# Optimization experiments

Hardware: AMD Instinct MI355X
Metric: run time of the kernel (lower is better)

Reference implementation:

```python
import jax, jax.numpy as jnp
import numpy as np

N_U = 50000; N_I = 50000; F = 128; H = 128; E = 800000; G = 512; C = 16; L = 3
EPS = 1e-5


def setup_inputs() -> dict:
    key = jax.random.key(0)
    ks = jax.random.split(key, 22)
    s = 1.0 / np.sqrt(H)
    inp = {}
    inp["x_user"] = jax.random.normal(ks[0], (N_U, F), jnp.float32)
    inp["x_item"] = jax.random.normal(ks[1], (N_I, F), jnp.float32)
    inp["edge_u2i"] = jnp.stack([jax.random.randint(ks[2], (E,), 0, N_U),
                                 jax.random.randint(ks[3], (E,), 0, N_I)])
    inp["edge_i2u"] = jnp.stack([jax.random.randint(ks[4], (E,), 0, N_I),
                                 jax.random.randint(ks[5], (E,), 0, N_U)])
    inp["batch_user"] = jnp.sort(jax.random.randint(ks[6], (N_U,), 0, G))
    inp["batch_item"] = jnp.sort(jax.random.randint(ks[7], (N_I,), 0, G))
    # GraphConv params per layer per relation (in-dim == hidden == 128, so stackable)
    inp["Wrel_u2i"] = jax.random.uniform(ks[8], (L, H, F), jnp.float32, -s, s)
    inp["Wroot_u2i"] = jax.random.uniform(ks[9], (L, H, F), jnp.float32, -s, s)
    inp["b_u2i"] = jax.random.uniform(ks[10], (L, H), jnp.float32, -s, s)
    inp["Wrel_i2u"] = jax.random.uniform(ks[11], (L, H, F), jnp.float32, -s, s)
    inp["Wroot_i2u"] = jax.random.uniform(ks[12], (L, H, F), jnp.float32, -s, s)
    inp["b_i2u"] = jax.random.uniform(ks[13], (L, H), jnp.float32, -s, s)
    # BatchNorm (one module per node type, reused across layers)
    inp["bn_g_user"] = jnp.ones((H,), jnp.float32)
    inp["bn_b_user"] = jnp.zeros((H,), jnp.float32)
    inp["bn_g_item"] = jnp.ones((H,), jnp.float32)
    inp["bn_b_item"] = jnp.zeros((H,), jnp.float32)
    # per-layer classifier heads
    inp["fc_W"] = jax.random.uniform(ks[14], (L, C, H), jnp.float32, -s, s)
    inp["fc_b"] = jax.random.uniform(ks[15], (L, C), jnp.float32, -s, s)
    return inp


def _graph_conv(x_src, x_dst, edge, Wrel, Wroot, b, n_dst):
    # GraphConv, aggr='add': W_rel @ sum_{j in N(i)} x_j + W_root @ x_i + b
    agg = jax.ops.segment_sum(x_src[edge[0]], edge[1], num_segments=n_dst)  # [n_dst, F]
    return agg @ Wrel.T + x_dst @ Wroot.T + b


def _bn(x, g, b):
    # BatchNorm1d over nodes, training-mode batch statistics (biased var)
    m = x.mean(0)
    v = jnp.mean((x - m) ** 2, axis=0)
    return (x - m) * jax.lax.rsqrt(v + EPS) * g + b


def reference(x_user, x_item, edge_u2i, edge_i2u, batch_user, batch_item,
              Wrel_u2i, Wroot_u2i, b_u2i, Wrel_i2u, Wroot_i2u, b_i2u,
              bn_g_user, bn_b_user, bn_g_item, bn_b_item, fc_W, fc_b):
    batch_all = jnp.concatenate([batch_user, batch_item])
    cnt = jax.ops.segment_sum(jnp.ones((N_U + N_I,), jnp.float32), batch_all,
                              num_segments=G)
    cnt = jnp.maximum(cnt, 1.0)[:, None]
    feats = []
    xu, xi = x_user, x_item
    for l in range(L):
        new_i = _graph_conv(xu, xi, edge_u2i, Wrel_u2i[l], Wroot_u2i[l], b_u2i[l], N_I)
        new_u = _graph_conv(xi, xu, edge_i2u, Wrel_i2u[l], Wroot_i2u[l], b_i2u[l], N_U)
        xu = _bn(jax.nn.relu(new_u), bn_g_user, bn_b_user)
        xi = _bn(jax.nn.relu(new_i), bn_g_item, bn_b_item)
        pooled = jax.ops.segment_sum(jnp.concatenate([xu, xi], 0), batch_all,
                                     num_segments=G) / cnt  # global mean pool [G, H]
        feats.append(pooled)
    feats = jnp.stack(feats)  # [L, G, H]
    # eval mode: F.dropout is identity; per-layer linear heads
    logits = jnp.einsum('lgh,lch->lgc', feats, fc_W) + fc_b[:, None, :]  # [L, G, C]
    return (logits, feats)
```

## Files before the change

### kernel.cpp

```cpp
#include <hip/hip_runtime.h>

#define NN 50000
#define FD 128
#define NE 800000
#define NG 512
#define NC 16
#define NL 3
#define NTOT 100000
#define NBLK 391
#define NBUCK 196
#define CAP 10240
#define BINTILE 2048
#define NBINBLK 782
#define BNEPS 1e-5f
#define LOGITS_N (NL*NG*NC)

typedef unsigned short u16;
typedef unsigned char u8;
typedef __attribute__((ext_vector_type(8))) short short8;
typedef __attribute__((ext_vector_type(4))) float f32x4;

#define OFF_GCNT     0ul
#define OFF_BCUR     4096ul
#define OFF_ACC      5120ul
#define MEMSET_BYTES 7168ul
#define OFF_USTART   7680ul
#define OFF_ISTART   10240ul
#define OFF_INVCNT   12800ul
#define OFF_BNSC     14848ul
#define OFF_BNSH     15872ul
#define OFF_ROWRANGE 16896ul
#define OFF_WB       817152ul
#define OFF_CSR      1210368ul
#define OFF_AGGI     9238528ul
#define OFF_AGGU     22038528ul
#define OFF_XU       34838528ul
#define OFF_XI       47638528ul
#define OFF_XU0      60438528ul
#define OFF_XI0      73238528ul

static __device__ __forceinline__ float bf2f(u16 v) {
  return __uint_as_float(((unsigned)v) << 16);
}
static __device__ __forceinline__ u16 f2bf(float f) {
  unsigned u = __float_as_uint(f);
  return (u16)((u + 0x7FFFu + ((u >> 16) & 1u)) >> 16);
}
static __device__ __forceinline__ void acc8(float* a, int4 v) {
  a[0] += __uint_as_float(((unsigned)v.x) << 16);
  a[1] += __uint_as_float(((unsigned)v.x) & 0xffff0000u);
  a[2] += __uint_as_float(((unsigned)v.y) << 16);
  a[3] += __uint_as_float(((unsigned)v.y) & 0xffff0000u);
  a[4] += __uint_as_float(((unsigned)v.z) << 16);
  a[5] += __uint_as_float(((unsigned)v.z) & 0xffff0000u);
  a[6] += __uint_as_float(((unsigned)v.w) << 16);
  a[7] += __uint_as_float(((unsigned)v.w) & 0xffff0000u);
}
static __device__ __forceinline__ void unp8(float* a, int4 v) {
  a[0] = __uint_as_float(((unsigned)v.x) << 16);
  a[1] = __uint_as_float(((unsigned)v.x) & 0xffff0000u);
  a[2] = __uint_as_float(((unsigned)v.y) << 16);
  a[3] = __uint_as_float(((unsigned)v.y) & 0xffff0000u);
  a[4] = __uint_as_float(((unsigned)v.z) << 16);
  a[5] = __uint_as_float(((unsigned)v.z) & 0xffff0000u);
  a[6] = __uint_as_float(((unsigned)v.w) << 16);
  a[7] = __uint_as_float(((unsigned)v.w) & 0xffff0000u);
}

__global__ __launch_bounds__(256) void k_hist_batch(const int* __restrict__ bu,
                                                    const int* __restrict__ bi,
                                                    int* __restrict__ gcnt) {
  int i = blockIdx.x*256 + threadIdx.x;
  if (i >= NTOT) return;
  int type = i >= NN;
  int g = type ? bi[i-NN] : bu[i];
  atomicAdd(&gcnt[type*NG + g], 1);
}

__global__ __launch_bounds__(512) void k_scan_g(const int* __restrict__ gcnt,
                                                int* __restrict__ ustart,
                                                int* __restrict__ istart,
                                                float* __restrict__ invcnt) {
  __shared__ int pu[512], pi[512];
  int t = threadIdx.x;
  int cu = gcnt[t], ci = gcnt[NG + t];
  pu[t] = cu; pi[t] = ci;
  __syncthreads();
  for (int off = 1; off < 512; off <<= 1) {
    int vu = (t >= off) ? pu[t-off] : 0;
    int vi = (t >= off) ? pi[t-off] : 0;
    __syncthreads();
    pu[t] += vu; pi[t] += vi;
    __syncthreads();
  }
  ustart[t] = pu[t] - cu;
  istart[t] = pi[t] - ci;
  if (t == 511) { ustart[NG] = pu[511]; istart[NG] = pi[511]; }
  int c = cu + ci;
  invcnt[t] = 1.0f / (float)(c > 0 ? c : 1);
}

__global__ __launch_bounds__(256) void k_bin(const int* __restrict__ eu2i,
                                             const int* __restrict__ ei2u,
                                             int* __restrict__ bcursor,
                                             int* __restrict__ binned) {
  __shared__ int hist[256];
  __shared__ int scan[256];
  __shared__ int gbase[256];
  __shared__ int rbuf[BINTILE];
  __shared__ u8 rbk[BINTILE];
  int tid = threadIdx.x;
  int base = blockIdx.x * BINTILE;
  hist[tid] = 0;
  __syncthreads();
  int packr[8], bkr[8], rankr[8];
  #pragma unroll
  for (int c = 0; c < 8; c++) {
    int idx = base + c*256 + tid;
    if (idx < 2*NE) {
      int rel = idx >= NE;
      int e = rel ? idx - NE : idx;
      const int* edge = rel ? ei2u : eu2i;
      int s = edge[e];
      int d = edge[NE + e];
      int slot = d + (rel ? NN : 0);
      int bk = slot >> 9;
      bkr[c] = bk;
      packr[c] = ((slot & 511) << 17) | s;
      rankr[c] = atomicAdd(&hist[bk], 1);
    } else bkr[c] = -1;
  }
  __syncthreads();
  scan[tid] = hist[tid];
  __syncthreads();
  for (int o = 1; o < 256; o <<= 1) {
    int v = (tid >= o) ? scan[tid - o] : 0;
    __syncthreads();
    scan[tid] += v;
    __syncthreads();
  }
  if (tid < NBUCK && hist[tid] > 0)
    gbase[tid] = atomicAdd(&bcursor[tid], hist[tid]);
  __syncthreads();
  #pragma unroll
  for (int c = 0; c < 8; c++) {
    if (bkr[c] >= 0) {
      int bk = bkr[c];
      int lpos = scan[bk] - hist[bk] + rankr[c];
      rbuf[lpos] = packr[c];
      rbk[lpos] = (u8)bk;
    }
  }
  __syncthreads();
  int nv = min(BINTILE, 2*NE - base);
  for (int j = tid; j < nv; j += 256) {
    int bk = rbk[j];
    int outpos = bk*CAP + gbase[bk] + (j - (scan[bk] - hist[bk]));
    binned[outpos] = rbuf[j];
  }
}

__global__ __launch_bounds__(256) void k_csrbuild(const int* __restrict__ bcursor,
                                                  int* __restrict__ csrbin,
                                                  int2* __restrict__ rowrange) {
  __shared__ int lcnt[512];
  __shared__ int scan2[256];
  __shared__ int lcsr[CAP];
  int b = blockIdx.x;
  int tid = threadIdx.x;
  int slot0 = b << 9;
  int nslots = min(512, NTOT - slot0);
  int n = bcursor[b];
  int gb = b * CAP;
  lcnt[tid] = 0; lcnt[tid + 256] = 0;
  __syncthreads();
  for (int i = tid; i < n; i += 256) {
    int e = csrbin[gb + i];
    atomicAdd(&lcnt[e >> 17], 1);
  }
  __syncthreads();
  int v0 = lcnt[2*tid], v1 = lcnt[2*tid + 1];
  int ps = v0 + v1;
  scan2[tid] = ps;
  __syncthreads();
  for (int o = 1; o < 256; o <<= 1) {
    int v = (tid >= o) ? scan2[tid - o] : 0;
    __syncthreads();
    scan2[tid] += v;
    __syncthreads();
  }
  int e0 = scan2[tid] - ps;
  int e1 = e0 + v0;
  if (2*tid < nslots)     rowrange[slot0 + 2*tid]     = make_int2(gb + e0, gb + e0 + v0);
  if (2*tid + 1 < nslots) rowrange[slot0 + 2*tid + 1] = make_int2(gb + e1, gb + e1 + v1);
  __syncthreads();
  lcnt[2*tid] = e0; lcnt[2*tid + 1] = e1;
  __syncthreads();
  for (int i = tid; i < n; i += 256) {
    int e = csrbin[gb + i];
    int pos = atomicAdd(&lcnt[e >> 17], 1);
    lcsr[pos] = e & 0x1FFFF;
  }
  __syncthreads();
  for (int i = tid; i < n; i += 256) csrbin[gb + i] = lcsr[i];
}

__global__ __launch_bounds__(256) void k_castX(const float* __restrict__ xu,
                                               const float* __restrict__ xi,
                                               u16* __restrict__ xbu,
                                               u16* __restrict__ xbi) {
  int b = blockIdx.x;
  int half = b >= 6250;
  const float* src = half ? xi : xu;
  u16* dst = half ? xbi : xbu;
  int i = ((half ? b - 6250 : b)*256 + threadIdx.x) * 4;
  float4 v = *(const float4*)(src + i);
  ushort4 o = { f2bf(v.x), f2bf(v.y), f2bf(v.z), f2bf(v.w) };
  *(ushort4*)(dst + i) = o;
}

__global__ __launch_bounds__(256) void k_castW(const float* __restrict__ WrelA,
                                               const float* __restrict__ WrootA,
                                               const float* __restrict__ WrelB,
                                               const float* __restrict__ WrootB,
                                               u16* __restrict__ WB) {
  int idx = blockIdx.x*256 + threadIdx.x;
  int lr = idx >> 15;
  int rem = idx & 32767;
  int h = rem >> 8;
  int k = rem & 255;
  int l = lr >> 1;
  int rel = lr & 1;
  const float* Wr = rel ? WrelB : WrelA;
  const float* Wo = rel ? WrootB : WrootA;
  float v = (k < FD) ? Wr[(l*FD + h)*FD + k] : Wo[(l*FD + h)*FD + (k-FD)];
  WB[idx] = f2bf(v);
}

__global__ __launch_bounds__(256) void k_gather(const u16* __restrict__ curU,
                                                const u16* __restrict__ curI,
                                                const int2* __restrict__ rowrange,
                                                const int* __restrict__ csr,
                                                u16* __restrict__ aggI,
                                                u16* __restrict__ aggU) {
  int b = blockIdx.x;
  int half = b >= 12500;
  int blk = half ? b - 12500 : b;
  const u16* src = half ? curI : curU;
  u16* out = half ? aggU : aggI;
  int slotbase = half ? NN : 0;
  int wid = __builtin_amdgcn_readfirstlane(threadIdx.x >> 6);
  int row = blk*4 + wid;
  int lane = threadIdx.x & 63;
  int q = lane >> 4;
  int c16 = (lane & 15) * 8;
  const u16* sp = src + c16;
  int2 pr = rowrange[slotbase + row];
  int p = pr.x, pe = pr.y;
  float a0[8], a1[8];
  #pragma unroll
  for (int j = 0; j < 8; j++) { a0[j] = 0.f; a1[j] = 0.f; }
  if (p + 8 <= pe) {
    int i0 = csr[p + q], i1 = csr[p + 4 + q];
    while (p + 16 <= pe) {
      int n0 = csr[p + 8 + q], n1 = csr[p + 12 + q];
      int4 v0 = *(const int4*)(sp + (size_t)i0*FD);
      int4 v1 = *(const int4*)(sp + (size_t)i1*FD);
      acc8(a0, v0); acc8(a1, v1);
      i0 = n0; i1 = n1; p += 8;
    }
    int4 v0 = *(const int4*)(sp + (size_t)i0*FD);
    int4 v1 = *(const int4*)(sp + (size_t)i1*FD);
    acc8(a0, v0); acc8(a1, v1);
    p += 8;
  }
  int rem = pe - p;
  if (q < rem) {
    int s = csr[p + q];
    acc8(a0, *(const int4*)(sp + (size_t)s*FD));
  }
  if (q + 4 < rem) {
    int s = csr[p + 4 + q];
    acc8(a1, *(const int4*)(sp + (size_t)s*FD));
  }
  #pragma unroll
  for (int j = 0; j < 8; j++) a0[j] += a1[j];
  #pragma unroll
  for (int j = 0; j < 8; j++) {
    a0[j] += __shfl_xor(a0[j], 16);
    a0[j] += __shfl_xor(a0[j], 32);
  }
  if (q == 0) {
    int4 o;
    o.x = (unsigned)f2bf(a0[0]) | ((unsigned)f2bf(a0[1]) << 16);
    o.y = (unsigned)f2bf(a0[2]) | ((unsigned)f2bf(a0[3]) << 16);
    o.z = (unsigned)f2bf(a0[4]) | ((unsigned)f2bf(a0[5]) << 16);
    o.w = (unsigned)f2bf(a0[6]) | ((unsigned)f2bf(a0[7]) << 16);
    *(int4*)(out + (size_t)row*FD + c16) = o;
  }
}

__global__ __launch_bounds__(256) void k_gemm(u16* __restrict__ aggU,
                                              u16* __restrict__ aggI,
                                              const u16* __restrict__ curU,
                                              const u16* __restrict__ curI,
                                              const u16* __restrict__ WBl,
                                              const float* __restrict__ bI2U,
                                              const float* __restrict__ bU2I,
                                              float* __restrict__ accSQ) {
  __shared__ u16 As[128*72];
  __shared__ u16 Bs[128*72];
  __shared__ float Sred[2][4][128];
  int ty = blockIdx.y;
  u16* A1 = ty ? aggI : aggU;
  const u16* A2 = ty ? curI : curU;
  const u16* WBp = ty ? WBl : (WBl + 32768);
  const float* bias = ty ? bU2I : bI2U;
  int tid = threadIdx.x;
  int n0 = blockIdx.x * 128;
  int w = __builtin_amdgcn_readfirstlane(tid >> 6);
  int lane = tid & 63;
  int l15 = lane & 15;
  int quad = lane >> 4;
  f32x4 acc[2][8];
  #pragma unroll
  for (int tr = 0; tr < 2; tr++)
    #pragma unroll
    for (int tc = 0; tc < 8; tc++)
      acc[tr][tc] = (f32x4){0.f,0.f,0.f,0.f};

  for (int ch = 0; ch < 4; ch++) {
    const u16* Ap = (ch < 2) ? ((const u16*)A1 + ch*64) : (A2 + (ch-2)*64);
    #pragma unroll
    for (int i = 0; i < 4; i++) {
      int e = i*256 + tid;
      int r = e >> 3, seg = e & 7;
      int4 v = {0,0,0,0};
      int gr = n0 + r;
      if (gr < NN) v = *(const int4*)(Ap + (size_t)gr*FD + seg*8);
      *(int4*)&As[r*72 + seg*8] = v;
    }
    #pragma unroll
    for (int i = 0; i < 4; i++) {
      int e = i*256 + tid;
      int r = e >> 3, seg = e & 7;
      int4 v = *(const int4*)(WBp + r*256 + ch*64 + seg*8);
      *(int4*)&Bs[r*72 + seg*8] = v;
    }
    __syncthreads();
    #pragma unroll
    for (int ks = 0; ks < 2; ks++) {
      int kb = ks*32 + quad*8;
      short8 af0 = *(const short8*)&As[(w*32 + l15)*72 + kb];
      short8 af1 = *(const short8*)&As[(w*32 + 16 + l15)*72 + kb];
      short8 bf[8];
      #pragma unroll
      for (int tc = 0; tc < 8; tc++)
        bf[tc] = *(const short8*)&Bs[(tc*16 + l15)*72 + kb];
      #pragma unroll
      for (int tc = 0; tc < 8; tc++) {
        acc[0][tc] = __builtin_amdgcn_mfma_f32_16x16x32_bf16(af0, bf[tc], acc[0][tc], 0, 0, 0);
        acc[1][tc] = __builtin_amdgcn_mfma_f32_16x16x32_bf16(af1, bf[tc], acc[1][tc], 0, 0, 0);
      }
    }
    __syncthreads();
  }
  float sv[8], qv[8], bj[8];
  #pragma unroll
  for (int tc = 0; tc < 8; tc++) {
    bj[tc] = bias[tc*16 + l15];
    sv[tc] = 0.f; qv[tc] = 0.f;
  }
  #pragma unroll
  for (int tr = 0; tr < 2; tr++) {
    int rbase = n0 + w*32 + tr*16 + quad*4;
    #pragma unroll
    for (int tc = 0; tc < 8; tc++) {
      int col = tc*16 + l15;
      #pragma unroll
      for (int g = 0; g < 4; g++) {
        int r = rbase + g;
        if (r < NN) {
          float v = acc[tr][tc][g] + bj[tc];
          float y = v > 0.f ? v : 0.f;
          sv[tc] += y; qv[tc] += y*y;
          A1[(size_t)r*FD + col] = f2bf(v);
        }
      }
    }
  }
  #pragma unroll
  for (int tc = 0; tc < 8; tc++) {
    sv[tc] += __shfl_xor(sv[tc], 16); qv[tc] += __shfl_xor(qv[tc], 16);
    sv[tc] += __shfl_xor(sv[tc], 32); qv[tc] += __shfl_xor(qv[tc], 32);
  }
  if (quad == 0) {
    #pragma unroll
    for (int tc = 0; tc < 8; tc++) {
      Sred[0][w][tc*16 + l15] = sv[tc];
      Sred[1][w][tc*16 + l15] = qv[tc];
    }
  }
  __syncthreads();
  if (tid < 128) {
    float s = Sred[0][0][tid] + Sred[0][1][tid] + Sred[0][2][tid] + Sred[0][3][tid];
    float q = Sred[1][0][tid] + Sred[1][1][tid] + Sred[1][2][tid] + Sred[1][3][tid];
    atomicAdd(&accSQ[ty*128 + tid], s);
    atomicAdd(&accSQ[256 + ty*128 + tid], q);
  }
}

__global__ __launch_bounds__(256) void k_bnfinal(float* __restrict__ accSQ,
                                                 const float* __restrict__ gu,
                                                 const float* __restrict__ bu,
                                                 const float* __restrict__ gi,
                                                 const float* __restrict__ bi,
                                                 float* __restrict__ bnsc,
                                                 float* __restrict__ bnsh) {
  int tid = threadIdx.x;
  int type = tid >> 7;
  int c = tid & 127;
  float s = accSQ[tid];
  float q = accSQ[256 + tid];
  accSQ[tid] = 0.f;
  accSQ[256 + tid] = 0.f;
  float inv = 1.0f / (float)NN;
  float mean = s * inv;
  float var = q * inv - mean*mean;
  float rstd = rsqrtf(var + BNEPS);
  float g = type ? gi[c] : gu[c];
  float bb = type ? bi[c] : bu[c];
  float sc = rstd * g;
  bnsc[tid] = sc;
  bnsh[tid] = bb - mean * sc;
}

__global__ __launch_bounds__(256) void k_bnpool(const u16* __restrict__ newU,
                                                const u16* __restrict__ newI,
                                                const int* __restrict__ ustart,
                                                const int* __restrict__ istart,
                                                const float* __restrict__ bnsc,
                                                const float* __restrict__ bnsh,
                                                const float* __restrict__ invcnt,
                                                u16* __restrict__ xu,
                                                u16* __restrict__ xi,
                                                float* __restrict__ feats) {
  __shared__ float red[16][128];
  int tid = threadIdx.x;
  int g = blockIdx.x;
  int rt = tid >> 4;
  int c8 = (tid & 15) * 8;
  float acc[8];
  #pragma unroll
  for (int j = 0; j < 8; j++) acc[j] = 0.f;
  #pragma unroll
  for (int type = 0; type < 2; type++) {
    const u16* in = type ? newI : newU;
    u16* out = type ? xi : xu;
    const int* st = type ? istart : ustart;
    int rs = st[g], re = st[g+1];
    float sc[8], sh[8];
    #pragma unroll
    for (int j = 0; j < 8; j++) {
      sc[j] = bnsc[type*128 + c8 + j];
      sh[j] = bnsh[type*128 + c8 + j];
    }
    int r = rs + rt;
    for (; r + 16 < re; r += 32) {
      int4 v0 = *(const int4*)(in + (size_t)r*FD + c8);
      int4 v1 = *(const int4*)(in + (size_t)(r+16)*FD + c8);
      float f0[8], f1[8];
      unp8(f0, v0); unp8(f1, v1);
      u16 ov[8];
      #pragma unroll
      for (int j = 0; j < 8; j++) {
        float y = f0[j] > 0.f ? f0[j] : 0.f;
        float o = y * sc[j] + sh[j];
        ov[j] = f2bf(o); acc[j] += o;
      }
      int4 ow;
      ow.x = (unsigned)ov[0] | ((unsigned)ov[1] << 16);
      ow.y = (unsigned)ov[2] | ((unsigned)ov[3] << 16);
      ow.z = (unsigned)ov[4] | ((unsigned)ov[5] << 16);
      ow.w = (unsigned)ov[6] | ((unsigned)ov[7] << 16);
      *(int4*)(out + (size_t)r*FD + c8) = ow;
      #pragma unroll
      for (int j = 0; j < 8; j++) {
        float y = f1[j] > 0.f ? f1[j] : 0.f;
        float o = y * sc[j] + sh[j];
        ov[j] = f2bf(o); acc[j] += o;
      }
      ow.x = (unsigned)ov[0] | ((unsigned)ov[1] << 16);
      ow.y = (unsigned)ov[2] | ((unsigned)ov[3] << 16);
      ow.z = (unsigned)ov[4] | ((unsigned)ov[5] << 16);
      ow.w = (unsigned)ov[6] | ((unsigned)ov[7] << 16);
      *(int4*)(out + (size_t)(r+16)*FD + c8) = ow;
    }
    for (; r < re; r += 16) {
      int4 v0 = *(const int4*)(in + (size_t)r*FD + c8);
      float f0[8];
      unp8(f0, v0);
      u16 ov[8];
      #pragma unroll
      for (int j = 0; j < 8; j++) {
        float y = f0[j] > 0.f ? f0[j] : 0.f;
        float o = y * sc[j] + sh[j];
        ov[j] = f2bf(o); acc[j] += o;
      }
      int4 ow;
      ow.x = (unsigned)ov[0] | ((unsigned)ov[1] << 16);
      ow.y = (unsigned)ov[2] | ((unsigned)ov[3] << 16);
      ow.z = (unsigned)ov[4] | ((unsigned)ov[5] << 16);
      ow.w = (unsigned)ov[6] | ((unsigned)ov[7] << 16);
      *(int4*)(out + (size_t)r*FD + c8) = ow;
    }
  }
  #pragma unroll
  for (int j = 0; j < 8; j++) red[rt][c8 + j] = acc[j];
  __syncthreads();
  if (tid < 128) {
    float s = 0.f;
    #pragma unroll
    for (int i = 0; i < 16; i++) s += red[i][tid];
    feats[(size_t)g*FD + tid] = s * invcnt[g];
  }
}

__global__ __launch_bounds__(256) void k_heads(const float* __restrict__ feats,
                                               const float* __restrict__ fcW,
                                               const float* __restrict__ fcb,
                                               float* __restrict__ logits) {
  int idx = blockIdx.x*256 + threadIdx.x;
  if (idx >= LOGITS_N) return;
  int l = idx >> 13;
  int rem = idx & 8191;
  int g = rem >> 4;
  int c = rem & 15;
  const float* f = feats + ((size_t)l*NG + g)*FD;
  const float* w = fcW + ((size_t)l*NC + c)*FD;
  float s = 0.f;
  #pragma unroll
  for (int k = 0; k < FD; k += 4) {
    float4 fv = *(const float4*)(f + k);
    float4 wv = *(const float4*)(w + k);
    s += fv.x*wv.x + fv.y*wv.y + fv.z*wv.z + fv.w*wv.w;
  }
  logits[idx] = s + fcb[l*NC + c];
}

extern "C" void kernel_launch(void* const* d_in, const int* in_sizes, int n_in,
                              void* d_out, int out_size, void* d_ws, size_t ws_size,
                              hipStream_t stream) {
  const float* x_user   = (const float*)d_in[0];
  const float* x_item   = (const float*)d_in[1];
  const int*   eu2i     = (const int*)d_in[2];
  const int*   ei2u     = (const int*)d_in[3];
  const int*   bu       = (const int*)d_in[4];
  const int*   bi       = (const int*)d_in[5];
  const float* Wrel_u2i = (const float*)d_in[6];
  const float* Wroot_u2i= (const float*)d_in[7];
  const float* b_u2i    = (const float*)d_in[8];
  const float* Wrel_i2u = (const float*)d_in[9];
  const float* Wroot_i2u= (const float*)d_in[10];
  const float* b_i2u    = (const float*)d_in[11];
  const float* bn_g_user= (const float*)d_in[12];
  const float* bn_b_user= (const float*)d_in[13];
  const float* bn_g_item= (const float*)d_in[14];
  const float* bn_b_item= (const float*)d_in[15];
  const float* fcW      = (const float*)d_in[16];
  const float* fcb      = (const float*)d_in[17];

  char* ws = (char*)d_ws;
  int*   gcnt   = (int*)(ws + OFF_GCNT);
  int*   bcursor= (int*)(ws + OFF_BCUR);
  float* accSQ  = (float*)(ws + OFF_ACC);
  int*   ustart = (int*)(ws + OFF_USTART);
  int*   istart = (int*)(ws + OFF_ISTART);
  float* invcnt = (float*)(ws + OFF_INVCNT);
  float* bnsc   = (float*)(ws + OFF_BNSC);
  float* bnsh   = (float*)(ws + OFF_BNSH);
  int2*  rowrange = (int2*)(ws + OFF_ROWRANGE);
  u16*   WB     = (u16*)(ws + OFF_WB);
  int*   csrbin = (int*)(ws + OFF_CSR);
  u16*   aggI   = (u16*)(ws + OFF_AGGI);
  u16*   aggU   = (u16*)(ws + OFF_AGGU);
  u16*   xu     = (u16*)(ws + OFF_XU);
  u16*   xi     = (u16*)(ws + OFF_XI);
  u16*   xu0    = (u16*)(ws + OFF_XU0);
  u16*   xi0    = (u16*)(ws + OFF_XI0);
  float* fout   = (float*)d_out;
  float* featsAll = fout + LOGITS_N;

  hipMemsetAsync(ws, 0, MEMSET_BYTES, stream);
  k_hist_batch<<<NBLK, 256, 0, stream>>>(bu, bi, gcnt);
  k_bin<<<NBINBLK, 256, 0, stream>>>(eu2i, ei2u, bcursor, csrbin);
  k_scan_g<<<1, 512, 0, stream>>>(gcnt, ustart, istart, invcnt);
  k_csrbuild<<<NBUCK, 256, 0, stream>>>(bcursor, csrbin, rowrange);
  k_castX<<<12500, 256, 0, stream>>>(x_user, x_item, xu0, xi0);
  k_castW<<<768, 256, 0, stream>>>(Wrel_u2i, Wroot_u2i, Wrel_i2u, Wroot_i2u, WB);

  const u16* curU = xu0;
  const u16* curI = xi0;
  for (int l = 0; l < NL; l++) {
    k_gather<<<25000, 256, 0, stream>>>(curU, curI, rowrange, csrbin, aggI, aggU);
    k_gemm<<<dim3(NBLK,2), 256, 0, stream>>>(aggU, aggI, curU, curI,
                                             WB + (size_t)l*2*32768,
                                             b_i2u + l*FD, b_u2i + l*FD,
                                             accSQ);
    k_bnfinal<<<1, 256, 0, stream>>>(accSQ, bn_g_user, bn_b_user,
                                     bn_g_item, bn_b_item, bnsc, bnsh);
    k_bnpool<<<NG, 256, 0, stream>>>(aggU, aggI, ustart, istart, bnsc, bnsh,
                                     invcnt, xu, xi,
                                     featsAll + (size_t)l*NG*FD);
    curU = xu; curI = xi;
  }
  k_heads<<<96, 256, 0, stream>>>(featsAll, fcW, fcb, fout);
}
```

Measured before the change: 515.7 us.

## Fuse neighbor gather into GEMM, fold BN finalize and heads into pooling

The CSR gather-sum is merged into the MFMA GEMM kernel. Each 64-row block aggregates its neighbor rows straight into shared memory, so the aggregated tensor no longer makes a round trip through global memory. The BN finalize step moves into the pooling kernel, using per-layer accumulator slots so no reset is needed, and the classifier heads are computed per graph in the same kernel. This removes several launches and one full global write plus read of the aggregated features per layer. In exchange, gather latency now serialises ahead of the GEMM inside each block, and the root-term A operand is read directly from global memory.

Result: slower. 561.0 us (+8.8%).

```diff
diff --git a/kernel.cpp b/kernel.cpp
--- a/kernel.cpp
+++ b/kernel.cpp
@@ -8,6 +8,7 @@
 #define NL 3
 #define NTOT 100000
 #define NBLK 391
+#define NGG 782
 #define NBUCK 196
 #define CAP 10240
 #define BINTILE 2048
@@ -23,21 +24,19 @@
 #define OFF_GCNT     0ul
 #define OFF_BCUR     4096ul
 #define OFF_ACC      5120ul
-#define MEMSET_BYTES 7168ul
-#define OFF_USTART   7680ul
-#define OFF_ISTART   10240ul
-#define OFF_INVCNT   12800ul
-#define OFF_BNSC     14848ul
-#define OFF_BNSH     15872ul
-#define OFF_ROWRANGE 16896ul
-#define OFF_WB       817152ul
-#define OFF_CSR      1210368ul
-#define OFF_AGGI     9238528ul
-#define OFF_AGGU     22038528ul
-#define OFF_XU       34838528ul
-#define OFF_XI       47638528ul
-#define OFF_XU0      60438528ul
-#define OFF_XI0      73238528ul
+#define MEMSET_BYTES 11264ul
+#define OFF_USTART   11776ul
+#define OFF_ISTART   14336ul
+#define OFF_INVCNT   16896ul
+#define OFF_ROWRANGE 19456ul
+#define OFF_WB       819712ul
+#define OFF_CSR      1213440ul
+#define OFF_AGGI     9241600ul
+#define OFF_AGGU     22041600ul
+#define OFF_XU       34841600ul
+#define OFF_XI       47641600ul
+#define OFF_XU0      60441600ul
+#define OFF_XI0      73241600ul
 
 static __device__ __forceinline__ float bf2f(u16 v) {
   return __uint_as_float(((unsigned)v) << 16);
@@ -237,109 +236,92 @@
   WB[idx] = f2bf(v);
 }
 
-__global__ __launch_bounds__(256) void k_gather(const u16* __restrict__ curU,
-                                                const u16* __restrict__ curI,
-                                                const int2* __restrict__ rowrange,
-                                                const int* __restrict__ csr,
-                                                u16* __restrict__ aggI,
-                                                u16* __restrict__ aggU) {
-  int b = blockIdx.x;
-  int half = b >= 12500;
-  int blk = half ? b - 12500 : b;
-  const u16* src = half ? curI : curU;
-  u16* out = half ? aggU : aggI;
-  int slotbase = half ? NN : 0;
-  int wid = __builtin_amdgcn_readfirstlane(threadIdx.x >> 6);
-  int row = blk*4 + wid;
-  int lane = threadIdx.x & 63;
-  int q = lane >> 4;
-  int c16 = (lane & 15) * 8;
-  const u16* sp = src + c16;
-  int2 pr = rowrange[slotbase + row];
-  int p = pr.x, pe = pr.y;
-  float a0[8], a1[8];
-  #pragma unroll
-  for (int j = 0; j < 8; j++) { a0[j] = 0.f; a1[j] = 0.f; }
-  if (p + 8 <= pe) {
-    int i0 = csr[p + q], i1 = csr[p + 4 + q];
-    while (p + 16 <= pe) {
-      int n0 = csr[p + 8 + q], n1 = csr[p + 12 + q];
-      int4 v0 = *(const int4*)(sp + (size_t)i0*FD);
-      int4 v1 = *(const int4*)(sp + (size_t)i1*FD);
-      acc8(a0, v0); acc8(a1, v1);
-      i0 = n0; i1 = n1; p += 8;
-    }
-    int4 v0 = *(const int4*)(sp + (size_t)i0*FD);
-    int4 v1 = *(const int4*)(sp + (size_t)i1*FD);
-    acc8(a0, v0); acc8(a1, v1);
-    p += 8;
-  }
-  int rem = pe - p;
-  if (q < rem) {
-    int s = csr[p + q];
-    acc8(a0, *(const int4*)(sp + (size_t)s*FD));
-  }
-  if (q + 4 < rem) {
-    int s = csr[p + 4 + q];
-    acc8(a1, *(const int4*)(sp + (size_t)s*FD));
-  }
-  #pragma unroll
-  for (int j = 0; j < 8; j++) a0[j] += a1[j];
-  #pragma unroll
-  for (int j = 0; j < 8; j++) {
-    a0[j] += __shfl_xor(a0[j], 16);
-    a0[j] += __shfl_xor(a0[j], 32);
-  }
-  if (q == 0) {
-    int4 o;
-    o.x = (unsigned)f2bf(a0[0]) | ((unsigned)f2bf(a0[1]) << 16);
-    o.y = (unsigned)f2bf(a0[2]) | ((unsigned)f2bf(a0[3]) << 16);
-    o.z = (unsigned)f2bf(a0[4]) | ((unsigned)f2bf(a0[5]) << 16);
-    o.w = (unsigned)f2bf(a0[6]) | ((unsigned)f2bf(a0[7]) << 16);
-    *(int4*)(out + (size_t)row*FD + c16) = o;
-  }
-}
-
-__global__ __launch_bounds__(256) void k_gemm(u16* __restrict__ aggU,
-                                              u16* __restrict__ aggI,
-                                              const u16* __restrict__ curU,
-                                              const u16* __restrict__ curI,
-                                              const u16* __restrict__ WBl,
-                                              const float* __restrict__ bI2U,
-                                              const float* __restrict__ bU2I,
-                                              float* __restrict__ accSQ) {
-  __shared__ u16 As[128*72];
+__global__ __launch_bounds__(256, 4) void k_gg(u16* __restrict__ aggU,
+                                               u16* __restrict__ aggI,
+                                               const u16* __restrict__ curU,
+                                               const u16* __restrict__ curI,
+                                               const int2* __restrict__ rowrange,
+                                               const int* __restrict__ csr,
+                                               const u16* __restrict__ WBl,
+                                               const float* __restrict__ bI2U,
+                                               const float* __restrict__ bU2I,
+                                               float* __restrict__ accSQ) {
+  __shared__ u16 As[64*136];
   __shared__ u16 Bs[128*72];
   __shared__ float Sred[2][4][128];
   int ty = blockIdx.y;
-  u16* A1 = ty ? aggI : aggU;
+  const u16* gsrc = ty ? curU : curI;
+  int slotbase = ty ? 0 : NN;
   const u16* A2 = ty ? curI : curU;
   const u16* WBp = ty ? WBl : (WBl + 32768);
   const float* bias = ty ? bU2I : bI2U;
+  u16* out = ty ? aggI : aggU;
+
   int tid = threadIdx.x;
-  int n0 = blockIdx.x * 128;
   int w = __builtin_amdgcn_readfirstlane(tid >> 6);
   int lane = tid & 63;
   int l15 = lane & 15;
-  int quad = lane >> 4;
-  f32x4 acc[2][8];
-  #pragma unroll
-  for (int tr = 0; tr < 2; tr++)
-    #pragma unroll
-    for (int tc = 0; tc < 8; tc++)
-      acc[tr][tc] = (f32x4){0.f,0.f,0.f,0.f};
-
+  int q = lane >> 4;
+  int n0 = blockIdx.x * 64;
+  int c16 = l15 * 8;
+  const u16* sp = gsrc + c16;
+
+  for (int rr = 0; rr < 16; rr++) {
+    int row = n0 + w*16 + rr;
+    float a0[8], a1[8];
+    #pragma unroll
+    for (int j = 0; j < 8; j++) { a0[j] = 0.f; a1[j] = 0.f; }
+    if (row < NN) {
+      int2 pr = rowrange[slotbase + row];
+      int p = pr.x, pe = pr.y;
+      if (p + 8 <= pe) {
+        int i0 = csr[p + q], i1 = csr[p + 4 + q];
+        while (p + 16 <= pe) {
+          int m0 = csr[p + 8 + q], m1 = csr[p + 12 + q];
+          int4 v0 = *(const int4*)(sp + (size_t)i0*FD);
+          int4 v1 = *(const int4*)(sp + (size_t)i1*FD);
+          acc8(a0, v0); acc8(a1, v1);
+          i0 = m0; i1 = m1; p += 8;
+        }
+        int4 v0 = *(const int4*)(sp + (size_t)i0*FD);
+        int4 v1 = *(const int4*)(sp + (size_t)i1*FD);
+        acc8(a0, v0); acc8(a1, v1);
+        p += 8;
+      }
+      int rem = pe - p;
+      if (q < rem) {
+        int s = csr[p + q];
+        acc8(a0, *(const int4*)(sp + (size_t)s*FD));
+      }
+      if (q + 4 < rem) {
+        int s = csr[p + 4 + q];
+        acc8(a1, *(const int4*)(sp + (size_t)s*FD));
+      }
+    }
+    #pragma unroll
+    for (int j = 0; j < 8; j++) a0[j] += a1[j];
+    #pragma unroll
+    for (int j = 0; j < 8; j++) {
+      a0[j] += __shfl_xor(a0[j], 16);
+      a0[j] += __shfl_xor(a0[j], 32);
+    }
+    if (q == 0) {
+      int4 o;
+      o.x = (unsigned)f2bf(a0[0]) | ((unsigned)f2bf(a0[1]) << 16);
+      o.y = (unsigned)f2bf(a0[2]) | ((unsigned)f2bf(a0[3]) << 16);
+      o.z = (unsigned)f2bf(a0[4]) | ((unsigned)f2bf(a0[5]) << 16);
+      o.w = (unsigned)f2bf(a0[6]) | ((unsigned)f2bf(a0[7]) << 16);
+      *(int4*)&As[(w*16 + rr)*136 + c16] = o;
+    }
+  }
+
+  f32x4 acc[8];
+  #pragma unroll
+  for (int tc = 0; tc < 8; tc++) acc[tc] = (f32x4){0.f,0.f,0.f,0.f};
+  int arow = n0 + w*16 + l15;
+  bool arok = arow < NN;
   for (int ch = 0; ch < 4; ch++) {
-    const u16* Ap = (ch < 2) ? ((const u16*)A1 + ch*64) : (A2 + (ch-2)*64);
-    #pragma unroll
-    for (int i = 0; i < 4; i++) {
-      int e = i*256 + tid;
-      int r = e >> 3, seg = e & 7;
-      int4 v = {0,0,0,0};
-      int gr = n0 + r;
-      if (gr < NN) v = *(const int4*)(Ap + (size_t)gr*FD + seg*8);
-      *(int4*)&As[r*72 + seg*8] = v;
-    }
+    if (ch) __syncthreads();
     #pragma unroll
     for (int i = 0; i < 4; i++) {
       int e = i*256 + tid;
@@ -350,42 +332,40 @@
     __syncthreads();
     #pragma unroll
     for (int ks = 0; ks < 2; ks++) {
-      int kb = ks*32 + quad*8;
-      short8 af0 = *(const short8*)&As[(w*32 + l15)*72 + kb];
-      short8 af1 = *(const short8*)&As[(w*32 + 16 + l15)*72 + kb];
-      short8 bf[8];
-      #pragma unroll
-      for (int tc = 0; tc < 8; tc++)
-        bf[tc] = *(const short8*)&Bs[(tc*16 + l15)*72 + kb];
+      int kb = ks*32 + q*8;
+      short8 af;
+      if (ch < 2) {
+        af = *(const short8*)&As[(w*16 + l15)*136 + ch*64 + kb];
+      } else {
+        af = (short8){0,0,0,0,0,0,0,0};
+        if (arok) af = *(const short8*)(A2 + (size_t)arow*FD + (ch-2)*64 + kb);
+      }
       #pragma unroll
       for (int tc = 0; tc < 8; tc++) {
-        acc[0][tc] = __builtin_amdgcn_mfma_f32_16x16x32_bf16(af0, bf[tc], acc[0][tc], 0, 0, 0);
-        acc[1][tc] = __builtin_amdgcn_mfma_f32_16x16x32_bf16(af1, bf[tc], acc[1][tc], 0, 0, 0);
-      }
-    }
-    __syncthreads();
-  }
+        short8 bf = *(const short8*)&Bs[(tc*16 + l15)*72 + kb];
+        acc[tc] = __builtin_amdgcn_mfma_f32_16x16x32_bf16(af, bf, acc[tc], 0, 0, 0);
+      }
+    }
+  }
+
   float sv[8], qv[8], bj[8];
   #pragma unroll
   for (int tc = 0; tc < 8; tc++) {
     bj[tc] = bias[tc*16 + l15];
     sv[tc] = 0.f; qv[tc] = 0.f;
   }
-  #pragma unroll
-  for (int tr = 0; tr < 2; tr++) {
-    int rbase = n0 + w*32 + tr*16 + quad*4;
-    #pragma unroll
-    for (int tc = 0; tc < 8; tc++) {
-      int col = tc*16 + l15;
-      #pragma unroll
-      for (int g = 0; g < 4; g++) {
-        int r = rbase + g;
-        if (r < NN) {
-          float v = acc[tr][tc][g] + bj[tc];
-          float y = v > 0.f ? v : 0.f;
-          sv[tc] += y; qv[tc] += y*y;
-          A1[(size_t)r*FD + col] = f2bf(v);
-        }
+  int rbase = n0 + w*16 + q*4;
+  #pragma unroll
+  for (int tc = 0; tc < 8; tc++) {
+    int col = tc*16 + l15;
+    #pragma unroll
+    for (int g = 0; g < 4; g++) {
+      int r = rbase + g;
+      if (r < NN) {
+        float v = acc[tc][g] + bj[tc];
+        float y = v > 0.f ? v : 0.f;
+        sv[tc] += y; qv[tc] += y*y;
+        out[(size_t)r*FD + col] = f2bf(v);
       }
     }
   }
@@ -394,7 +374,7 @@
     sv[tc] += __shfl_xor(sv[tc], 16); qv[tc] += __shfl_xor(qv[tc], 16);
     sv[tc] += __shfl_xor(sv[tc], 32); qv[tc] += __shfl_xor(qv[tc], 32);
   }
-  if (quad == 0) {
+  if (q == 0) {
     #pragma unroll
     for (int tc = 0; tc < 8; tc++) {
       Sred[0][w][tc*16 + l15] = sv[tc];
@@ -404,50 +384,49 @@
   __syncthreads();
   if (tid < 128) {
     float s = Sred[0][0][tid] + Sred[0][1][tid] + Sred[0][2][tid] + Sred[0][3][tid];
-    float q = Sred[1][0][tid] + Sred[1][1][tid] + Sred[1][2][tid] + Sred[1][3][tid];
+    float qq = Sred[1][0][tid] + Sred[1][1][tid] + Sred[1][2][tid] + Sred[1][3][tid];
     atomicAdd(&accSQ[ty*128 + tid], s);
-    atomicAdd(&accSQ[256 + ty*128 + tid], q);
-  }
-}
-
-__global__ __launch_bounds__(256) void k_bnfinal(float* __restrict__ accSQ,
-                                                 const float* __restrict__ gu,
-                                                 const float* __restrict__ bu,
-                                                 const float* __restrict__ gi,
-                                                 const float* __restrict__ bi,
-                                                 float* __restrict__ bnsc,
-                                                 float* __restrict__ bnsh) {
-  int tid = threadIdx.x;
-  int type = tid >> 7;
-  int c = tid & 127;
-  float s = accSQ[tid];
-  float q = accSQ[256 + tid];
-  accSQ[tid] = 0.f;
-  accSQ[256 + tid] = 0.f;
-  float inv = 1.0f / (float)NN;
-  float mean = s * inv;
-  float var = q * inv - mean*mean;
-  float rstd = rsqrtf(var + BNEPS);
-  float g = type ? gi[c] : gu[c];
-  float bb = type ? bi[c] : bu[c];
-  float sc = rstd * g;
-  bnsc[tid] = sc;
-  bnsh[tid] = bb - mean * sc;
+    atomicAdd(&accSQ[256 + ty*128 + tid], qq);
+  }
 }
 
 __global__ __launch_bounds__(256) void k_bnpool(const u16* __restrict__ newU,
                                                 const u16* __restrict__ newI,
                                                 const int* __restrict__ ustart,
                                                 const int* __restrict__ istart,
-                                                const float* __restrict__ bnsc,
-                                                const float* __restrict__ bnsh,
+                                                const float* __restrict__ accSQ,
+                                                const float* __restrict__ gu,
+                                                const float* __restrict__ bu,
+                                                const float* __restrict__ gi,
+                                                const float* __restrict__ bi,
                                                 const float* __restrict__ invcnt,
                                                 u16* __restrict__ xu,
                                                 u16* __restrict__ xi,
-                                                float* __restrict__ feats) {
+                                                float* __restrict__ feats,
+                                                const float* __restrict__ fcWl,
+                                                const float* __restrict__ fcbl,
+                                                float* __restrict__ logitsl) {
   __shared__ float red[16][128];
+  __shared__ float ssc[256], ssh[256];
+  __shared__ float sfeat[128];
   int tid = threadIdx.x;
   int g = blockIdx.x;
+  {
+    int type = tid >> 7;
+    int c = tid & 127;
+    float s = accSQ[tid];
+    float qq = accSQ[256 + tid];
+    float inv = 1.0f / (float)NN;
+    float mean = s * inv;
+    float var = qq * inv - mean*mean;
+    float rstd = rsqrtf(var + BNEPS);
+    float gg = type ? gi[c] : gu[c];
+    float bb = type ? bi[c] : bu[c];
+    float sc = rstd * gg;
+    ssc[tid] = sc;
+    ssh[tid] = bb - mean * sc;
+  }
+  __syncthreads();
   int rt = tid >> 4;
   int c8 = (tid & 15) * 8;
   float acc[8];
@@ -456,14 +435,14 @@
   #pragma unroll
   for (int type = 0; type < 2; type++) {
     const u16* in = type ? newI : newU;
-    u16* out = type ? xi : xu;
+    u16* outp = type ? xi : xu;
     const int* st = type ? istart : ustart;
     int rs = st[g], re = st[g+1];
     float sc[8], sh[8];
     #pragma unroll
     for (int j = 0; j < 8; j++) {
-      sc[j] = bnsc[type*128 + c8 + j];
-      sh[j] = bnsh[type*128 + c8 + j];
+      sc[j] = ssc[type*128 + c8 + j];
+      sh[j] = ssh[type*128 + c8 + j];
     }
     int r = rs + rt;
     for (; r + 16 < re; r += 32) {
@@ -483,7 +462,7 @@
       ow.y = (unsigned)ov[2] | ((unsigned)ov[3] << 16);
       ow.z = (unsigned)ov[4] | ((unsigned)ov[5] << 16);
       ow.w = (unsigned)ov[6] | ((unsigned)ov[7] << 16);
-      *(int4*)(out + (size_t)r*FD + c8) = ow;
+      *(int4*)(outp + (size_t)r*FD + c8) = ow;
       #pragma unroll
       for (int j = 0; j < 8; j++) {
         float y = f1[j] > 0.f ? f1[j] : 0.f;
@@ -494,7 +473,7 @@
       ow.y = (unsigned)ov[2] | ((unsigned)ov[3] << 16);
       ow.z = (unsigned)ov[4] | ((unsigned)ov[5] << 16);
       ow.w = (unsigned)ov[6] | ((unsigned)ov[7] << 16);
-      *(int4*)(out + (size_t)(r+16)*FD + c8) = ow;
+      *(int4*)(outp + (size_t)(r+16)*FD + c8) = ow;
     }
     for (; r < re; r += 16) {
       int4 v0 = *(const int4*)(in + (size_t)r*FD + c8);
@@ -512,7 +491,7 @@
       ow.y = (unsigned)ov[2] | ((unsigned)ov[3] << 16);
       ow.z = (unsigned)ov[4] | ((unsigned)ov[5] << 16);
       ow.w = (unsigned)ov[6] | ((unsigned)ov[7] << 16);
-      *(int4*)(out + (size_t)r*FD + c8) = ow;
+      *(int4*)(outp + (size_t)r*FD + c8) = ow;
     }
   }
   #pragma unroll
@@ -522,30 +501,23 @@
     float s = 0.f;
     #pragma unroll
     for (int i = 0; i < 16; i++) s += red[i][tid];
-    feats[(size_t)g*FD + tid] = s * invcnt[g];
-  }
-}
-
-__global__ __launch_bounds__(256) void k_heads(const float* __restrict__ feats,
-                                               const float* __restrict__ fcW,
-                                               const float* __restrict__ fcb,
-                                               float* __restrict__ logits) {
-  int idx = blockIdx.x*256 + threadIdx.x;
-  if (idx >= LOGITS_N) return;
-  int l = idx >> 13;
-  int rem = idx & 8191;
-  int g = rem >> 4;
-  int c = rem & 15;
-  const float* f = feats + ((size_t)l*NG + g)*FD;
-  const float* w = fcW + ((size_t)l*NC + c)*FD;
-  float s = 0.f;
-  #pragma unroll
-  for (int k = 0; k < FD; k += 4) {
-    float4 fv = *(const float4*)(f + k);
-    float4 wv = *(const float4*)(w + k);
-    s += fv.x*wv.x + fv.y*wv.y + fv.z*wv.z + fv.w*wv.w;
-  }
-  logits[idx] = s + fcb[l*NC + c];
+    float f = s * invcnt[g];
+    sfeat[tid] = f;
+    feats[(size_t)g*FD + tid] = f;
+  }
+  __syncthreads();
+  if (tid < 128) {
+    int c = tid >> 3, u = tid & 7;
+    const float* wv = fcWl + c*FD + u*16;
+    const float* fv = sfeat + u*16;
+    float s = 0.f;
+    #pragma unroll
+    for (int j = 0; j < 16; j++) s += wv[j] * fv[j];
+    s += __shfl_xor(s, 1);
+    s += __shfl_xor(s, 2);
+    s += __shfl_xor(s, 4);
+    if (u == 0) logitsl[g*NC + c] = s + fcbl[c];
+  }
 }
 
 extern "C" void kernel_launch(void* const* d_in, const int* in_sizes, int n_in,
@@ -577,8 +549,6 @@
   int*   ustart = (int*)(ws + OFF_USTART);
   int*   istart = (int*)(ws + OFF_ISTART);
   float* invcnt = (float*)(ws + OFF_INVCNT);
-  float* bnsc   = (float*)(ws + OFF_BNSC);
-  float* bnsh   = (float*)(ws + OFF_BNSH);
   int2*  rowrange = (int2*)(ws + OFF_ROWRANGE);
   u16*   WB     = (u16*)(ws + OFF_WB);
   int*   csrbin = (int*)(ws + OFF_CSR);
@@ -602,17 +572,16 @@
   const u16* curU = xu0;
   const u16* curI = xi0;
   for (int l = 0; l < NL; l++) {
-    k_gather<<<25000, 256, 0, stream>>>(curU, curI, rowrange, csrbin, aggI, aggU);
-    k_gemm<<<dim3(NBLK,2), 256, 0, stream>>>(aggU, aggI, curU, curI,
-                                             WB + (size_t)l*2*32768,
-                                             b_i2u + l*FD, b_u2i + l*FD,
-                                             accSQ);
-    k_bnfinal<<<1, 256, 0, stream>>>(accSQ, bn_g_user, bn_b_user,
-                                     bn_g_item, bn_b_item, bnsc, bnsh);
-    k_bnpool<<<NG, 256, 0, stream>>>(aggU, aggI, ustart, istart, bnsc, bnsh,
+    k_gg<<<dim3(NGG,2), 256, 0, stream>>>(aggU, aggI, curU, curI, rowrange, csrbin,
+                                          WB + (size_t)l*2*32768,
+                                          b_i2u + l*FD, b_u2i + l*FD,
+                                          accSQ + l*512);
+    k_bnpool<<<NG, 256, 0, stream>>>(aggU, aggI, ustart, istart, accSQ + l*512,
+                                     bn_g_user, bn_b_user, bn_g_item, bn_b_item,
                                      invcnt, xu, xi,
-                                     featsAll + (size_t)l*NG*FD);
+                                     featsAll + (size_t)l*NG*FD,
+                                     fcW + (size_t)l*NC*FD, fcb + l*NC,
+                                     fout + (size_t)l*NG*NC);
     curU = xu; curI = xi;
   }
-  k_heads<<<96, 256, 0, stream>>>(featsAll, fcW, fcb, fout);
-}
+}
```
